# Kernel tuning notes

Measured on AMD Instinct MI355X. Metric: run time of the kernel, lower is better.

## Reference

```python
import jax, jax.numpy as jnp
import numpy as np

K = 3          # kernel_size
G = 16         # group_number
BN_EPS = 1e-3  # keras BatchNormalization default epsilon


def setup_inputs() -> dict:
    key = jax.random.key(0)
    ks = jax.random.split(key, 4)
    B, H, W, C = 8, 64, 64, 256
    R = 4  # reduction_ratio
    return {
        "x": jax.random.normal(ks[0], (B, H, W, C), dtype=jnp.float32),
        "W1": jax.random.normal(ks[1], (C, C // R), dtype=jnp.float32) * 0.05,
        "b1": jnp.zeros((C // R,), dtype=jnp.float32),
        "gamma": jnp.ones((C // R,), dtype=jnp.float32),
        "beta": jnp.zeros((C // R,), dtype=jnp.float32),
        "mov_mean": jnp.zeros((C // R,), dtype=jnp.float32),
        "mov_var": jnp.ones((C // R,), dtype=jnp.float32),
        "W2": jax.random.normal(ks[2], (C // R, K * K * G), dtype=jnp.float32) * 0.05,
        "b2": jnp.zeros((K * K * G,), dtype=jnp.float32),
    }


def reference(x, W1, b1, gamma, beta, mov_mean, mov_var, W2, b2):
    B, H, W, C = x.shape
    # kernel generation: 1x1 conv -> BN (inference) -> ReLU -> 1x1 conv
    h = jnp.einsum("bhwc,cd->bhwd", x, W1) + b1
    h = (h - mov_mean) * (gamma / jnp.sqrt(mov_var + BN_EPS)) + beta
    h = jax.nn.relu(h)
    kernel = jnp.einsum("bhwd,de->bhwe", h, W2) + b2      # (B,H,W,K*K*G)
    kernel = kernel.reshape(B, H, W, K * K, 1, G)
    # extract_patches (SAME, stride 1): tf orders last axis as (ki,kj,channel)
    p = K // 2
    xp = jnp.pad(x, ((0, 0), (p, p), (p, p), (0, 0)))
    patches = jnp.stack(
        [xp[:, i:i + H, j:j + W, :] for i in range(K) for j in range(K)],
        axis=3,
    )  # (B,H,W,K*K,C)
    patches = patches.reshape(B, H, W, K * K, C // G, G)
    out = jnp.sum(kernel * patches, axis=3)               # (B,H,W,C//G,G)
    out = out.reshape(B, H, W, C)
    return out, kernel
```

## Files before the change

kernel.cpp:

```cpp
#include <hip/hip_runtime.h>
#include <hip/hip_bf16.h>

typedef __attribute__((ext_vector_type(8))) short bf16x8;
typedef __attribute__((ext_vector_type(4))) float f32x4;

#define NPIX 32768

__device__ __forceinline__ ushort f2bf(float f) {
    __hip_bfloat16 h = __float2bfloat16(f);
    ushort u; __builtin_memcpy(&u, &h, 2);
    return u;
}

__global__ __launch_bounds__(512, 1) void fused_kernel(
        const float* __restrict__ x,
        const float* __restrict__ W1, const float* __restrict__ b1,
        const float* __restrict__ gamma, const float* __restrict__ beta,
        const float* __restrict__ mean, const float* __restrict__ var,
        const float* __restrict__ W2, const float* __restrict__ b2,
        float* __restrict__ ker, float* __restrict__ out) {
    __shared__ __align__(16) char smem[133120];
    const int t = threadIdx.x;
    const int wv = t >> 6, ln = t & 63;
    char* arena = smem + wv * 10240;
    char* w1s   = smem + 81920;
    char* w2s   = smem + 114688;
    const int bid = (int)blockIdx.x;
    const int img = bid & 7;
    const int rp  = bid >> 3;
    const int i   = rp * 2 + (wv >> 2);
    const int lb  = img * 64 + i;
    const int j0  = (wv & 3) * 16;
    const int pw  = lb * 64 + j0;
    const int r16 = ln & 15, g = ln >> 4;

    #pragma unroll
    for (int m = 0; m < 4; m++) {
        int idx = m * 512 + t;
        int ln2 = idx & 63, dt = (idx >> 6) & 3, kk = idx >> 8;
        int d = dt * 16 + (ln2 & 15);
        float sc = gamma[d] * rsqrtf(var[d] + 1e-3f);
        int cbase = kk * 32 + (ln2 >> 4) * 8;
        ushort tmp[8];
        #pragma unroll
        for (int cc = 0; cc < 8; cc++)
            tmp[cc] = f2bf(W1[(cbase + cc) * 64 + d] * sc);
        __builtin_memcpy(w1s + idx * 16, tmp, 16);
    }
    #pragma unroll
    for (int m = 0; m < 3; m++) {
        int idx = m * 512 + t;
        if (idx < 1152) {
            int ln2 = idx & 63, rem = idx >> 6;
            int et = rem % 9, kk = rem / 9;
            int e = et * 16 + (ln2 & 15);
            int dbase = kk * 32 + (ln2 >> 4) * 8;
            ushort tmp[8];
            #pragma unroll
            for (int cc = 0; cc < 8; cc++)
                tmp[cc] = f2bf(W2[(dbase + cc) * 144 + e]);
            __builtin_memcpy(w2s + idx * 16, tmp, 16);
        }
    }
    float b1fv[4];
    #pragma unroll
    for (int dt = 0; dt < 4; dt++) {
        int d = dt * 16 + r16;
        float sc = gamma[d] * rsqrtf(var[d] + 1e-3f);
        b1fv[dt] = (b1[d] - mean[d]) * sc + beta[d];
    }

    __syncthreads();

    {
        const float4* xg = (const float4*)(x + (size_t)pw * 256);
        #pragma unroll
        for (int it = 0; it < 16; it++) {
            float4 v = xg[it * 64 + ln];
            ushort4 b4; b4.x = f2bf(v.x); b4.y = f2bf(v.y);
            b4.z = f2bf(v.z); b4.w = f2bf(v.w);
            int bcol = (ln * 8) ^ ((it & 7) << 4);
            *(ushort4*)(arena + it * 512 + bcol) = b4;
        }
    }

    const f32x4* xv4 = (const f32x4*)x;
    const f32x4 z4 = {0.f, 0.f, 0.f, 0.f};
    f32x4 wa[3], wb[3], wc[3], wd[3];
    #pragma unroll
    for (int r = 0; r < 3; r++) {
        int row = i + r - 1;
        bool rv = (unsigned)row < 64u;
        const size_t rb = (size_t)(lb + r - 1) * 64;
        wa[r] = (rv && j0 > 0) ? xv4[(rb + (j0 - 1)) * 64 + ln] : z4;
        wb[r] = rv ? xv4[(rb + j0) * 64 + ln] : z4;
        wc[r] = rv ? xv4[(rb + j0 + 1) * 64 + ln] : z4;
        wd[r] = rv ? xv4[(rb + j0 + 2) * 64 + ln] : z4;
    }

    f32x4 acc[4];
    #pragma unroll
    for (int dt = 0; dt < 4; dt++) {
        float bv = b1fv[dt];
        acc[dt] = (f32x4){bv, bv, bv, bv};
    }
    #pragma unroll
    for (int kk = 0; kk < 8; kk++) {
        int bcA = (kk * 64 + g * 16) ^ ((r16 & 7) << 4);
        bf16x8 av = *(const bf16x8*)(arena + r16 * 512 + bcA);
        #pragma unroll
        for (int dt = 0; dt < 4; dt++) {
            bf16x8 bv = *(const bf16x8*)(w1s + (((kk * 4 + dt) << 6) + ln) * 16);
            acc[dt] = __builtin_amdgcn_mfma_f32_16x16x32_bf16(av, bv, acc[dt], 0, 0, 0);
        }
    }

    #pragma unroll
    for (int dt = 0; dt < 4; dt++) {
        #pragma unroll
        for (int r = 0; r < 4; r++) {
            int q = g * 4 + r;
            int bcol = ((dt * 16 + r16) * 2) ^ ((q & 7) << 4);
            *(ushort*)(arena + 8192 + q * 128 + bcol) = f2bf(fmaxf(acc[dt][r], 0.f));
        }
    }

    f32x4 acc2[9];
    #pragma unroll
    for (int et = 0; et < 9; et++) {
        float bv = b2[et * 16 + r16];
        acc2[et] = (f32x4){bv, bv, bv, bv};
    }
    #pragma unroll
    for (int kk = 0; kk < 2; kk++) {
        int bcA = (kk * 64 + g * 16) ^ ((r16 & 7) << 4);
        bf16x8 av = *(const bf16x8*)(arena + 8192 + r16 * 128 + bcA);
        #pragma unroll
        for (int et = 0; et < 9; et++) {
            bf16x8 bv = *(const bf16x8*)(w2s + (((kk * 9 + et) << 6) + ln) * 16);
            acc2[et] = __builtin_amdgcn_mfma_f32_16x16x32_bf16(av, bv, acc2[et], 0, 0, 0);
        }
    }

    float* ksf = (float*)arena;
    #pragma unroll
    for (int et = 0; et < 9; et++) {
        #pragma unroll
        for (int r = 0; r < 4; r++) {
            int q = g * 4 + r;
            ksf[q * 148 + et * 16 + r16] = acc2[et][r];
        }
    }

    const int s4 = (ln & 3) * 4;
    #pragma unroll 4
    for (int pp = 0; pp < 16; pp++) {
        const int j = j0 + pp;
        const float* kp = ksf + pp * 148 + s4;
        f32x4 o = {0.f, 0.f, 0.f, 0.f};
        #pragma unroll
        for (int r = 0; r < 3; r++) {
            o += (*(const f32x4*)(kp + (r * 3 + 0) * 16)) * wa[r];
            o += (*(const f32x4*)(kp + (r * 3 + 1) * 16)) * wb[r];
            o += (*(const f32x4*)(kp + (r * 3 + 2) * 16)) * wc[r];
        }
        __builtin_nontemporal_store(o, &((f32x4*)out)[(size_t)(lb * 64 + j) * 64 + ln]);
        #pragma unroll
        for (int r = 0; r < 3; r++) { wa[r] = wb[r]; wb[r] = wc[r]; wc[r] = wd[r]; }
        if (pp < 14) {
            const int jn = j + 3;
            const bool cv = jn < 64;
            #pragma unroll
            for (int r = 0; r < 3; r++) {
                int row = i + r - 1;
                bool rv = (unsigned)row < 64u;
                wd[r] = (rv && cv)
                    ? xv4[((size_t)(lb + r - 1) * 64 + jn) * 64 + ln] : z4;
            }
        }
    }

    {
        float* kerW = ker + (size_t)pw * 144;
        #pragma unroll
        for (int m = 0; m < 9; m++) {
            int fidx = m * 64 + ln;
            int row  = fidx / 36;
            int col4 = fidx - row * 36;
            f32x4 v = *(const f32x4*)(ksf + row * 148 + col4 * 4);
            __builtin_nontemporal_store(v, (f32x4*)(kerW + fidx * 4));
        }
    }
}

extern "C" void kernel_launch(void* const* d_in, const int* in_sizes, int n_in,
                              void* d_out, int out_size, void* d_ws, size_t ws_size,
                              hipStream_t stream) {
    const float* x     = (const float*)d_in[0];
    const float* W1    = (const float*)d_in[1];
    const float* b1    = (const float*)d_in[2];
    const float* gamma = (const float*)d_in[3];
    const float* beta  = (const float*)d_in[4];
    const float* mmean = (const float*)d_in[5];
    const float* mvar  = (const float*)d_in[6];
    const float* W2    = (const float*)d_in[7];
    const float* b2    = (const float*)d_in[8];

    float* out_main = (float*)d_out;
    float* out_ker  = (float*)d_out + 8388608;

    fused_kernel<<<NPIX / 128, 512, 0, stream>>>(
        x, W1, b1, gamma, beta, mmean, mvar, W2, b2, out_ker, out_main);
}
```

Measured before the change: 21.46 us.

## Coalesce weight staging with float4 loads and defer window loads past GEMM

Weight staging now reads W1 and W2 as contiguous float4 vectors and scatters bf16 values into the MFMA-ready LDS layout, replacing strided scalar global reads. The barrier moves after the x tile staging so that the weight and activation loads overlap, and the first GEMM and ReLU now run before the 3x3 window registers are loaded. This should cut latency from uncoalesced weight reads and register pressure during the GEMM. In exchange, the scattered 2-byte LDS stores may cause bank conflicts, and the window loads now sit in the critical path after the GEMM.

Measured after the change: 24.49 us. 1.14x slower.

```diff
diff --git a/kernel.cpp b/kernel.cpp
--- a/kernel.cpp
+++ b/kernel.cpp
@@ -34,32 +34,49 @@
     const int pw  = lb * 64 + j0;
     const int r16 = ln & 15, g = ln >> 4;
 
-    #pragma unroll
-    for (int m = 0; m < 4; m++) {
-        int idx = m * 512 + t;
-        int ln2 = idx & 63, dt = (idx >> 6) & 3, kk = idx >> 8;
-        int d = dt * 16 + (ln2 & 15);
-        float sc = gamma[d] * rsqrtf(var[d] + 1e-3f);
-        int cbase = kk * 32 + (ln2 >> 4) * 8;
-        ushort tmp[8];
-        #pragma unroll
-        for (int cc = 0; cc < 8; cc++)
-            tmp[cc] = f2bf(W1[(cbase + cc) * 64 + d] * sc);
-        __builtin_memcpy(w1s + idx * 16, tmp, 16);
-    }
-    #pragma unroll
-    for (int m = 0; m < 3; m++) {
-        int idx = m * 512 + t;
-        if (idx < 1152) {
-            int ln2 = idx & 63, rem = idx >> 6;
-            int et = rem % 9, kk = rem / 9;
-            int e = et * 16 + (ln2 & 15);
-            int dbase = kk * 32 + (ln2 >> 4) * 8;
-            ushort tmp[8];
-            #pragma unroll
-            for (int cc = 0; cc < 8; cc++)
-                tmp[cc] = f2bf(W2[(dbase + cc) * 144 + e]);
-            __builtin_memcpy(w2s + idx * 16, tmp, 16);
+    {
+        const int dq = t & 15;
+        const int dtq = dq >> 2;
+        const int rbase = (dq & 3) * 4;
+        float sc4[4];
+        #pragma unroll
+        for (int j = 0; j < 4; j++) {
+            int d = dq * 4 + j;
+            sc4[j] = gamma[d] * rsqrtf(var[d] + 1e-3f);
+        }
+        const float4* w1v = (const float4*)W1;
+        ushort* w1u = (ushort*)w1s;
+        #pragma unroll
+        for (int m = 0; m < 8; m++) {
+            int f = m * 512 + t;
+            int c = f >> 4;
+            int kk = c >> 5, c3 = (c >> 3) & 3, cc = c & 7;
+            float4 v = w1v[f];
+            int base = ((((kk * 4 + dtq) << 6) + (c3 << 4) + rbase) << 3) + cc;
+            w1u[base]      = f2bf(v.x * sc4[0]);
+            w1u[base + 8]  = f2bf(v.y * sc4[1]);
+            w1u[base + 16] = f2bf(v.z * sc4[2]);
+            w1u[base + 24] = f2bf(v.w * sc4[3]);
+        }
+    }
+    {
+        const float4* w2v = (const float4*)W2;
+        ushort* w2u = (ushort*)w2s;
+        #pragma unroll
+        for (int m = 0; m < 5; m++) {
+            int f = m * 512 + t;
+            if (f < 2304) {
+                int dcol = f / 36, eq = f - dcol * 36;
+                int kk = dcol >> 5, c3 = (dcol >> 3) & 3, cc = dcol & 7;
+                float4 v = w2v[f];
+                float va[4]; *(float4*)va = v;
+                #pragma unroll
+                for (int j = 0; j < 4; j++) {
+                    int e = eq * 4 + j;
+                    int et = e >> 4, r = e & 15;
+                    w2u[((((kk * 9 + et) << 6) + (c3 << 4) + r) << 3) + cc] = f2bf(va[j]);
+                }
+            }
         }
     }
     float b1fv[4];
@@ -69,8 +86,6 @@
         float sc = gamma[d] * rsqrtf(var[d] + 1e-3f);
         b1fv[dt] = (b1[d] - mean[d]) * sc + beta[d];
     }
-
-    __syncthreads();
 
     {
         const float4* xg = (const float4*)(x + (size_t)pw * 256);
@@ -81,6 +96,34 @@
             b4.z = f2bf(v.z); b4.w = f2bf(v.w);
             int bcol = (ln * 8) ^ ((it & 7) << 4);
             *(ushort4*)(arena + it * 512 + bcol) = b4;
+        }
+    }
+    __syncthreads();
+
+    f32x4 acc[4];
+    #pragma unroll
+    for (int dt = 0; dt < 4; dt++) {
+        float bv = b1fv[dt];
+        acc[dt] = (f32x4){bv, bv, bv, bv};
+    }
+    #pragma unroll
+    for (int kk = 0; kk < 8; kk++) {
+        int bcA = (kk * 64 + g * 16) ^ ((r16 & 7) << 4);
+        bf16x8 av = *(const bf16x8*)(arena + r16 * 512 + bcA);
+        #pragma unroll
+        for (int dt = 0; dt < 4; dt++) {
+            bf16x8 bv = *(const bf16x8*)(w1s + (((kk * 4 + dt) << 6) + ln) * 16);
+            acc[dt] = __builtin_amdgcn_mfma_f32_16x16x32_bf16(av, bv, acc[dt], 0, 0, 0);
+        }
+    }
+
+    #pragma unroll
+    for (int dt = 0; dt < 4; dt++) {
+        #pragma unroll
+        for (int r = 0; r < 4; r++) {
+            int q = g * 4 + r;
+            int bcol = ((dt * 16 + r16) * 2) ^ ((q & 7) << 4);
+            *(ushort*)(arena + 8192 + q * 128 + bcol) = f2bf(fmaxf(acc[dt][r], 0.f));
         }
     }
 
@@ -96,33 +139,6 @@
         wb[r] = rv ? xv4[(rb + j0) * 64 + ln] : z4;
         wc[r] = rv ? xv4[(rb + j0 + 1) * 64 + ln] : z4;
         wd[r] = rv ? xv4[(rb + j0 + 2) * 64 + ln] : z4;
-    }
-
-    f32x4 acc[4];
-    #pragma unroll
-    for (int dt = 0; dt < 4; dt++) {
-        float bv = b1fv[dt];
-        acc[dt] = (f32x4){bv, bv, bv, bv};
-    }
-    #pragma unroll
-    for (int kk = 0; kk < 8; kk++) {
-        int bcA = (kk * 64 + g * 16) ^ ((r16 & 7) << 4);
-        bf16x8 av = *(const bf16x8*)(arena + r16 * 512 + bcA);
-        #pragma unroll
-        for (int dt = 0; dt < 4; dt++) {
-            bf16x8 bv = *(const bf16x8*)(w1s + (((kk * 4 + dt) << 6) + ln) * 16);
-            acc[dt] = __builtin_amdgcn_mfma_f32_16x16x32_bf16(av, bv, acc[dt], 0, 0, 0);
-        }
-    }
-
-    #pragma unroll
-    for (int dt = 0; dt < 4; dt++) {
-        #pragma unroll
-        for (int r = 0; r < 4; r++) {
-            int q = g * 4 + r;
-            int bcol = ((dt * 16 + r16) * 2) ^ ((q & 7) << 4);
-            *(ushort*)(arena + 8192 + q * 128 + bcol) = f2bf(fmaxf(acc[dt][r], 0.f));
-        }
     }
 
     f32x4 acc2[9];
```
